# Performance work log

Measured on AMD Instinct MI355X. Metric: run time of the kernel, lower is better.

Reference implementation:

```python
import jax, jax.numpy as jnp
import numpy as np

B, S, HID = 1, 2048, 4096
H = 32
Q_LORA, KV_LORA = 1536, 512
NOPE, ROPE, VDIM = 128, 64, 128
EPS = 1e-6
ROPE_BASE = 10000.0


def rms_norm(x, w, eps=EPS):
    var = jnp.mean(x.astype(jnp.float32) ** 2, axis=-1, keepdims=True)
    return (x * jax.lax.rsqrt(var + eps)).astype(x.dtype) * w


def rope_cos_sin(position_ids, dim=ROPE):
    inv_freq = 1.0 / (ROPE_BASE ** (jnp.arange(0, dim, 2, dtype=jnp.float32) / dim))
    ang = position_ids.astype(jnp.float32)[..., None] * inv_freq  # [B,S,dim/2]
    return jnp.cos(ang), jnp.sin(ang)


def apply_rope(x, cos, sin):
    # x: [..., dim]; neox-style rotate_half on the rope slice
    d2 = x.shape[-1] // 2
    x1, x2 = x[..., :d2], x[..., d2:]
    return jnp.concatenate([x1 * cos - x2 * sin, x2 * cos + x1 * sin], axis=-1)


def setup_inputs() -> dict:
    key = jax.random.key(0)
    ks = jax.random.split(key, 8)
    s = 0.02
    return {
        "position_ids": jnp.broadcast_to(jnp.arange(S, dtype=jnp.int32), (B, S)),
        "hidden_states": jax.random.normal(ks[0], (B, S, HID), jnp.float32),
        "w_fused_a": jax.random.normal(ks[1], (Q_LORA + KV_LORA + ROPE, HID), jnp.float32) * s,
        "q_a_ln_w": jnp.ones((Q_LORA,), jnp.float32),
        "kv_a_ln_w": jnp.ones((KV_LORA,), jnp.float32),
        "w_q_b": jax.random.normal(ks[2], (H * (NOPE + ROPE), Q_LORA), jnp.float32) * s,
        "w_kv_b": jax.random.normal(ks[3], (H * 2 * NOPE, KV_LORA), jnp.float32) * s,
        "w_o": jax.random.normal(ks[4], (HID, H * VDIM), jnp.float32) * s,
    }


def reference(position_ids, hidden_states, w_fused_a, q_a_ln_w, kv_a_ln_w, w_q_b, w_kv_b, w_o):
    # fused A projection: -> [q_lora | kv_lora | rope]
    a = jnp.einsum('bsh,oh->bso', hidden_states, w_fused_a)
    cq = rms_norm(a[..., :Q_LORA], q_a_ln_w)
    ckv = rms_norm(a[..., Q_LORA:Q_LORA + KV_LORA], kv_a_ln_w)
    k_pe = a[..., Q_LORA + KV_LORA:]  # [B,S,ROPE], shared across heads

    # Q up-projection, split nope/rope per head
    q = jnp.einsum('bsr,or->bso', cq, w_q_b).reshape(B, S, H, NOPE + ROPE)
    q_nope, q_pe = q[..., :NOPE], q[..., NOPE:]

    # KV up-projection: per head [k_nope | v]
    kv = jnp.einsum('bsr,or->bso', ckv, w_kv_b).reshape(B, S, H, 2 * NOPE)
    k_nope, v = kv[..., :NOPE], kv[..., NOPE:]

    # RoPE on the rope slices only
    cos, sin = rope_cos_sin(position_ids)  # [B,S,ROPE/2]
    q_pe = apply_rope(q_pe, cos[:, :, None, :], sin[:, :, None, :])
    k_pe = apply_rope(k_pe, cos, sin)

    qf = jnp.concatenate([q_nope, q_pe], axis=-1)  # [B,S,H,NOPE+ROPE]
    kf = jnp.concatenate([k_nope, jnp.broadcast_to(k_pe[:, :, None, :], (B, S, H, ROPE))], axis=-1)

    scale = 1.0 / np.sqrt(NOPE + ROPE)
    scores = jnp.einsum('bshd,bthd->bhst', qf, kf) * scale
    causal = jnp.tril(jnp.ones((S, S), dtype=bool))
    scores = jnp.where(causal, scores, jnp.finfo(scores.dtype).min)
    p = jax.nn.softmax(scores, axis=-1)
    attn = jnp.einsum('bhst,bthd->bshd', p, v).reshape(B, S, H * VDIM)
    return jnp.einsum('bsd,od->bso', attn, w_o)
```

## Files before the change

### kernel.cpp

```cpp
#include <hip/hip_runtime.h>
#include <cmath>

#define S_LEN 2048
#define HID 4096
#define NHEAD 32
#define Q_LORA 1536
#define KV_LORA 512
#define NOPE 128
#define ROPE_D 64
#define VDIM 128
#define QK_DIM 192
#define FUSED_N 2112
#define FUSED_NPAD 2304

typedef __attribute__((ext_vector_type(8))) short short8;
typedef __attribute__((ext_vector_type(4))) float floatx4;
typedef unsigned short ushort_t;

__device__ inline short f2bf(float f) {
    union { float f; unsigned u; } v; v.f = f;
    unsigned r = (v.u + 0x7fffu + ((v.u >> 16) & 1u)) >> 16;
    return (short)r;
}
__device__ inline float bf2f(ushort_t u) {
    union { unsigned u; float f; } v; v.u = ((unsigned)u) << 16; return v.f;
}

#define GLOAD16(g, l)                                                        \
    __builtin_amdgcn_global_load_lds(                                        \
        (const __attribute__((address_space(1))) unsigned int*)(g),          \
        (__attribute__((address_space(3))) unsigned int*)(l), 16, 0, 0)

__device__ inline short8 conv8(const float* s) {
    const float4* s4 = (const float4*)s;
    float4 a = s4[0], b = s4[1];
    short8 v;
    v[0] = f2bf(a.x); v[1] = f2bf(a.y); v[2] = f2bf(a.z); v[3] = f2bf(a.w);
    v[4] = f2bf(b.x); v[5] = f2bf(b.y); v[6] = f2bf(b.z); v[7] = f2bf(b.w);
    return v;
}

#define CE0 (S_LEN * HID)
#define CE1 (CE0 + FUSED_NPAD * HID)
#define CE2 (CE1 + NHEAD * QK_DIM * Q_LORA)
#define CE3 (CE2 + NHEAD * 256 * KV_LORA)

__global__ __launch_bounds__(256) void conv_all(
    const float* __restrict__ hs, const float* __restrict__ w_a,
    const float* __restrict__ w_qb, const float* __restrict__ w_kvb,
    ushort_t* __restrict__ hs_bf, ushort_t* __restrict__ w_a_bf,
    ushort_t* __restrict__ w_qb_bf, ushort_t* __restrict__ w_kvb_bf)
{
    int i = (blockIdx.x * 256 + threadIdx.x) * 8;
    if (i < CE0) {
        *(short8*)(hs_bf + i) = conv8(hs + i);
    } else if (i < CE1) {
        int j = i - CE0;
        short8 v;
        if (j < FUSED_N * HID) v = conv8(w_a + j);
        else                   v = (short8){0,0,0,0,0,0,0,0};
        *(short8*)(w_a_bf + j) = v;
    } else if (i < CE2) {
        int j = i - CE1;
        *(short8*)(w_qb_bf + j) = conv8(w_qb + j);
    } else if (i < CE3) {
        int j = i - CE2;
        *(short8*)(w_kvb_bf + j) = conv8(w_kvb + j);
    }
}

__global__ __launch_bounds__(256) void conv_bf16(
    const float* __restrict__ src, ushort_t* __restrict__ dst, int n)
{
    int i = (blockIdx.x * 256 + threadIdx.x) * 8;
    if (i >= n) return;
    *(short8*)(dst + i) = conv8(src + i);
}

__global__ __launch_bounds__(256) void reduce_add_f32(
    const float* __restrict__ p0, const float* __restrict__ p1,
    float* __restrict__ o, int n)
{
    int i = (blockIdx.x * 256 + threadIdx.x) * 4;
    if (i >= n) return;
    float4 a = *(const float4*)(p0 + i);
    float4 b = *(const float4*)(p1 + i);
    float4 c; c.x = a.x + b.x; c.y = a.y + b.y; c.z = a.z + b.z; c.w = a.w + b.w;
    *(float4*)(o + i) = c;
}

__device__ __forceinline__ void gemm_pipe_body(
    const ushort_t* __restrict__ A, int lda,
    const ushort_t* __restrict__ B, int ldb,
    int m0, int n0, int kbeg, int nst,
    short8* LDS, floatx4 (&acc)[8][4], int tid)
{
    const int lane = tid & 63;
    const int wave = tid >> 6;
    const int m    = lane & 15;
    const int quad = lane >> 4;
    const int wr   = wave >> 2;
    const int wc   = wave & 3;

    auto stage = [&](int k0, int buf) {
        short8* dst = &LDS[buf * 2048];
        #pragma unroll
        for (int r = 0; r < 2; ++r) {
            int i  = tid + r * 512;
            int mi = i & 15, qd = (i >> 4) & 3, rb = i >> 6;
            GLOAD16(A + (size_t)(m0 + rb * 16 + mi) * lda + k0 + qd * 8, dst + i);
            GLOAD16(B + (size_t)(n0 + rb * 16 + mi) * ldb + k0 + qd * 8, dst + 1024 + i);
        }
    };

    stage(kbeg, 0);
    stage(kbeg + 32, 1);

    for (int i = 0; i < nst; ++i) {
        if (i + 2 < nst) {
            stage(kbeg + (i + 2) * 32, (i + 2) % 3);
            asm volatile("s_waitcnt vmcnt(8)" ::: "memory");
        } else if (i + 1 < nst) {
            asm volatile("s_waitcnt vmcnt(4)" ::: "memory");
        } else {
            asm volatile("s_waitcnt vmcnt(0)" ::: "memory");
        }
        asm volatile("s_barrier" ::: "memory");

        const short8* As = &LDS[(i % 3) * 2048];
        const short8* Bs = As + 1024;
        short8 af[8], bfr[4];
        #pragma unroll
        for (int ii = 0; ii < 8; ++ii)
            af[ii] = As[((wr * 8 + ii) * 4 + quad) * 16 + m];
        #pragma unroll
        for (int j = 0; j < 4; ++j)
            bfr[j] = Bs[((wc * 4 + j) * 4 + quad) * 16 + m];

        __builtin_amdgcn_s_setprio(1);
        #pragma unroll
        for (int ri = 0; ri < 8; ++ri)
            #pragma unroll
            for (int ci = 0; ci < 4; ++ci)
                acc[ri][ci] = __builtin_amdgcn_mfma_f32_16x16x32_bf16(
                    af[ri], bfr[ci], acc[ri][ci], 0, 0, 0);
        __builtin_amdgcn_s_setprio(0);

        asm volatile("s_barrier" ::: "memory");
    }
}

__device__ inline void store_c(float* p, float v)    { *p = v; }
__device__ inline void store_c(ushort_t* p, float v) { *p = (ushort_t)f2bf(v); }

template <typename CT>
__device__ __forceinline__ void gemm256_store(
    CT* __restrict__ C, int ldc, int N, int m0, int n0,
    floatx4 (&acc)[8][4], int tid)
{
    const int lane = tid & 63;
    const int wave = tid >> 6;
    const int m    = lane & 15;
    const int quad = lane >> 4;
    const int wr   = wave >> 2, wc = wave & 3;
    #pragma unroll
    for (int ci = 0; ci < 4; ++ci) {
        int col = n0 + wc * 64 + ci * 16 + m;
        if (col < N) {
            #pragma unroll
            for (int ri = 0; ri < 8; ++ri) {
                int row = m0 + wr * 128 + ri * 16 + quad * 4;
                #pragma unroll
                for (int r = 0; r < 4; ++r)
                    store_c(&C[(size_t)(row + r) * ldc + col], acc[ri][ci][r]);
            }
        }
    }
}

template <typename CT>
__global__ __launch_bounds__(512) void gemm256p(
    const ushort_t* __restrict__ A, int lda,
    const ushort_t* __restrict__ B, int ldb,
    CT* __restrict__ C, int ldc, int N, int Klen, int nx, int ny)
{
    __shared__ short8 LDS[3 * 2048];
    const int tid = threadIdx.x;

    const int nwg = gridDim.x;
    const int bid = blockIdx.x;
    const int wg  = (bid & 7) * (nwg >> 3) + (bid >> 3);
    const int nxy = nx * ny;
    const int z   = wg / nxy;
    const int rxy = wg - z * nxy;
    const int m0  = (rxy / nx) * 256;
    const int n0  = (rxy % nx) * 256;
    CT* Cz = C + (size_t)z * (size_t)ny * 256 * ldc;

    floatx4 acc[8][4];
    #pragma unroll
    for (int i = 0; i < 8; ++i)
        #pragma unroll
        for (int j = 0; j < 4; ++j) acc[i][j] = (floatx4){0.f, 0.f, 0.f, 0.f};

    gemm_pipe_body(A, lda, B, ldb, m0, n0, z * Klen, Klen >> 5, LDS, acc, tid);
    gemm256_store<CT>(Cz, ldc, N, m0, n0, acc, tid);
}

__global__ __launch_bounds__(512) void gemm34p(
    const ushort_t* __restrict__ a_bf,
    const ushort_t* __restrict__ w_qb_bf,
    const ushort_t* __restrict__ w_kvb_bf,
    ushort_t* __restrict__ q_bf,
    ushort_t* __restrict__ kv_bf)
{
    __shared__ short8 LDS[3 * 2048];
    const int tid = threadIdx.x;

    const int nwg = gridDim.x;
    const int bid = blockIdx.x;
    const int wg  = (bid & 7) * (nwg >> 3) + (bid >> 3);
    const int x   = wg % 56;
    const int m0  = (wg / 56) * 256;

    const ushort_t* A; const ushort_t* B; ushort_t* C;
    int ldb, ldc, N, K, n0;
    if (x < 24) {
        A = a_bf;            B = w_qb_bf;  C = q_bf;
        ldb = Q_LORA;        ldc = NHEAD * QK_DIM; N = NHEAD * QK_DIM;
        K = Q_LORA;          n0 = x * 256;
    } else {
        A = a_bf + Q_LORA;   B = w_kvb_bf; C = kv_bf;
        ldb = KV_LORA;       ldc = NHEAD * 256;    N = NHEAD * 256;
        K = KV_LORA;         n0 = (x - 24) * 256;
    }

    floatx4 acc[8][4];
    #pragma unroll
    for (int i = 0; i < 8; ++i)
        #pragma unroll
        for (int j = 0; j < 4; ++j) acc[i][j] = (floatx4){0.f, 0.f, 0.f, 0.f};

    gemm_pipe_body(A, FUSED_N, B, ldb, m0, n0, 0, K >> 5, LDS, acc, tid);
    gemm256_store<ushort_t>(C, ldc, N, m0, n0, acc, tid);
}

__global__ __launch_bounds__(256) void norm_rope_kernel(
    const float* __restrict__ part,
    ushort_t* __restrict__ a,
    const float* __restrict__ q_ln_w,
    const float* __restrict__ kv_ln_w,
    const int* __restrict__ pos_ids)
{
    const int s = blockIdx.x;
    const size_t PL = (size_t)S_LEN * FUSED_N;
    const float* r0 = part + (size_t)s * FUSED_N;
    ushort_t* row = a + (size_t)s * FUSED_N;
    __shared__ float red[256];
    const int tid = threadIdx.x;

    float vq[6];
    float ss = 0.f;
    #pragma unroll
    for (int j = 0; j < 6; ++j) {
        int i = tid + j * 256;
        vq[j] = (r0[i] + r0[i + PL]) + (r0[i + 2 * PL] + r0[i + 3 * PL]);
        ss += vq[j] * vq[j];
    }
    red[tid] = ss;
    __syncthreads();
    for (int w = 128; w > 0; w >>= 1) {
        if (tid < w) red[tid] += red[tid + w];
        __syncthreads();
    }
    float scale_q = rsqrtf(red[0] / (float)Q_LORA + 1e-6f);
    #pragma unroll
    for (int j = 0; j < 6; ++j) {
        int i = tid + j * 256;
        row[i] = (ushort_t)f2bf(vq[j] * scale_q * q_ln_w[i]);
    }
    __syncthreads();

    float vk[2];
    ss = 0.f;
    #pragma unroll
    for (int j = 0; j < 2; ++j) {
        int iw = tid + j * 256;
        int i  = Q_LORA + iw;
        vk[j] = (r0[i] + r0[i + PL]) + (r0[i + 2 * PL] + r0[i + 3 * PL]);
        ss += vk[j] * vk[j];
    }
    red[tid] = ss;
    __syncthreads();
    for (int w = 128; w > 0; w >>= 1) {
        if (tid < w) red[tid] += red[tid + w];
        __syncthreads();
    }
    float scale_kv = rsqrtf(red[0] / (float)KV_LORA + 1e-6f);
    #pragma unroll
    for (int j = 0; j < 2; ++j) {
        int iw = tid + j * 256;
        row[Q_LORA + iw] = (ushort_t)f2bf(vk[j] * scale_kv * kv_ln_w[iw]);
    }

    if (tid < 32) {
        const int j = tid;
        float pos = (float)pos_ids[s];
        float inv_freq = expf(-(float)j * (9.210340371976184f / 32.f));
        float ang = pos * inv_freq;
        float c = cosf(ang), sn = sinf(ang);
        int i1 = Q_LORA + KV_LORA + j;
        int i2 = i1 + 32;
        float x1 = (r0[i1] + r0[i1 + PL]) + (r0[i1 + 2 * PL] + r0[i1 + 3 * PL]);
        float x2 = (r0[i2] + r0[i2 + PL]) + (r0[i2 + 2 * PL] + r0[i2 + 3 * PL]);
        row[i1] = (ushort_t)f2bf(x1 * c - x2 * sn);
        row[i2] = (ushort_t)f2bf(x2 * c + x1 * sn);
    }
}

__global__ __launch_bounds__(256) void rope_q_kernel(
    ushort_t* __restrict__ q, const int* __restrict__ pos_ids)
{
    int idx = blockIdx.x * blockDim.x + threadIdx.x;
    if (idx >= S_LEN * NHEAD) return;
    int s = idx >> 5;
    float pos = (float)pos_ids[s];
    ushort_t* qp = q + (size_t)idx * QK_DIM + NOPE;
    #pragma unroll 4
    for (int j = 0; j < 32; ++j) {
        float inv_freq = expf(-(float)j * (9.210340371976184f / 32.f));
        float ang = pos * inv_freq;
        float c = cosf(ang), sn = sinf(ang);
        float x1 = bf2f(qp[j]), x2 = bf2f(qp[32 + j]);
        qp[j]      = (ushort_t)f2bf(x1 * c - x2 * sn);
        qp[32 + j] = (ushort_t)f2bf(x2 * c + x1 * sn);
    }
}

__global__ __launch_bounds__(256) void transpose_v(
    const ushort_t* __restrict__ kv, ushort_t* __restrict__ vt)
{
    __shared__ ushort_t vs[32][128];
    const int tid = threadIdx.x;
    const int h   = blockIdx.y;
    const int kb  = blockIdx.x;

    #pragma unroll
    for (int rep = 0; rep < 2; ++rep) {
        int i = rep * 256 + tid;
        int key = i >> 4, ch = i & 15;
        *(short8*)&vs[key][ch * 8] =
            *(const short8*)(kv + ((size_t)(kb * 32 + key) * NHEAD + h) * 256 + 128 + ch * 8);
    }
    __syncthreads();
    #pragma unroll
    for (int rep = 0; rep < 2; ++rep) {
        int i = rep * 256 + tid;
        int kq = i >> 7, d = i & 127;
        short8 v;
        #pragma unroll
        for (int j = 0; j < 8; ++j) v[j] = vs[kq * 8 + j][d];
        *(short8*)(vt + (((size_t)h * (S_LEN / 8) + kb * 4 + kq) * 128 + d) * 8) = v;
    }
}

__global__ __launch_bounds__(256) void attn_mfma(
    const ushort_t* __restrict__ q,
    const ushort_t* __restrict__ kv,
    const ushort_t* __restrict__ abuf,
    const ushort_t* __restrict__ vt,
    ushort_t* __restrict__ attn)
{
    __shared__ short8 KF[2][768];
    __shared__ short8 VF[2][512];
    __shared__ short8 PA[256];

    const int tid  = threadIdx.x;
    const int wave = tid >> 6;
    const int lane = tid & 63;
    const int m    = lane & 15;
    const int quad = lane >> 4;
    const int h    = blockIdx.y;
    const int pair = blockIdx.x;
    const int qtiles[2] = { 31 - pair, pair };

    const float scale = 0.07216878364870323f;
    short* pas = (short*)PA;

    auto stage_kv = [&](int t0, int buf) {
        #pragma unroll
        for (int rep = 0; rep < 3; ++rep) {
            int i   = rep * 256 + tid;
            int key = i & 31, qd = (i >> 5) & 3, c = i >> 7;
            if (c < 4)
                GLOAD16(kv + ((size_t)(t0 + key) * NHEAD + h) * 256 + c * 32 + qd * 8,
                        &KF[buf][i]);
            else
                GLOAD16(abuf + (size_t)(t0 + key) * FUSED_N + 2048 + (c - 4) * 32 + qd * 8,
                        &KF[buf][i]);
        }
        const ushort_t* vsrc = vt + ((size_t)h * (S_LEN / 8) + (t0 >> 3)) * 1024;
        GLOAD16(vsrc + (size_t)tid * 8, &VF[buf][tid]);
        GLOAD16(vsrc + (size_t)(256 + tid) * 8, &VF[buf][256 + tid]);
    };

    for (int qi = 0; qi < 2; ++qi) {
        const int q0 = qtiles[qi] * 64;
        const int qrow_base = q0 + wave * 16;

        short8 qf[6];
        {
            const ushort_t* qrow = q + ((size_t)(qrow_base + m) * NHEAD + h) * QK_DIM;
            #pragma unroll
            for (int c = 0; c < 6; ++c)
                qf[c] = *(const short8*)(qrow + c * 32 + quad * 8);
        }

        floatx4 O[8];
        #pragma unroll
        for (int t = 0; t < 8; ++t) O[t] = (floatx4){0.f, 0.f, 0.f, 0.f};
        float mrow[4] = {-1e30f, -1e30f, -1e30f, -1e30f};
        float lrow[4] = {0.f, 0.f, 0.f, 0.f};

        const int ntile = (q0 + 64) / 32;

        stage_kv(0, 0);
        __syncthreads();
        int cur = 0;

        for (int tt = 0; tt < ntile; ++tt) {
            const int t0 = tt * 32;
            if (tt + 1 < ntile) stage_kv(t0 + 32, cur ^ 1);

            floatx4 s0 = (floatx4){0.f, 0.f, 0.f, 0.f};
            floatx4 s1 = (floatx4){0.f, 0.f, 0.f, 0.f};
            const int kb = quad * 32 + m;
            __builtin_amdgcn_s_setprio(1);
            #pragma unroll
            for (int c = 0; c < 6; ++c) {
                s0 = __builtin_amdgcn_mfma_f32_16x16x32_bf16(qf[c], KF[cur][c * 128 + kb],      s0, 0, 0, 0);
                s1 = __builtin_amdgcn_mfma_f32_16x16x32_bf16(qf[c], KF[cur][c * 128 + kb + 16], s1, 0, 0, 0);
            }
            __builtin_amdgcn_s_setprio(0);

            const int qb = qrow_base + quad * 4;
            float sv0[4], sv1[4];
            #pragma unroll
            for (int r = 0; r < 4; ++r) {
                float a0 = s0[r] * scale;
                float a1 = s1[r] * scale;
                if (t0 + m > qb + r)      a0 = -1e30f;
                if (t0 + 16 + m > qb + r) a1 = -1e30f;
                sv0[r] = a0; sv1[r] = a1;
            }
            #pragma unroll
            for (int r = 0; r < 4; ++r) {
                float v = fmaxf(sv0[r], sv1[r]);
                v = fmaxf(v, __shfl_xor(v, 1));
                v = fmaxf(v, __shfl_xor(v, 2));
                v = fmaxf(v, __shfl_xor(v, 4));
                v = fmaxf(v, __shfl_xor(v, 8));
                if (v > mrow[r] + 8.f) {
                    float alpha = __expf(mrow[r] - v);
                    lrow[r] *= alpha;
                    #pragma unroll
                    for (int t = 0; t < 8; ++t) O[t][r] *= alpha;
                    mrow[r] = v;
                }
                float p0 = __expf(sv0[r] - mrow[r]);
                float p1 = __expf(sv1[r] - mrow[r]);
                lrow[r] += p0 + p1;
                int row = quad * 4 + r;
                short* pw = pas + wave * 512;
                pw[((m >> 3) + 0) * 128 + row * 8 + (m & 7)] = f2bf(p0);
                pw[((m >> 3) + 2) * 128 + row * 8 + (m & 7)] = f2bf(p1);
            }

            short8 pfrag = PA[wave * 64 + quad * 16 + m];
            __builtin_amdgcn_s_setprio(1);
            #pragma unroll
            for (int t = 0; t < 8; ++t) {
                O[t] = __builtin_amdgcn_mfma_f32_16x16x32_bf16(
                    pfrag, VF[cur][quad * 128 + m + 16 * t], O[t], 0, 0, 0);
            }
            __builtin_amdgcn_s_setprio(0);

            __syncthreads();
            cur ^= 1;
        }

        #pragma unroll
        for (int r = 0; r < 4; ++r) {
            float l = lrow[r];
            l += __shfl_xor(l, 1);
            l += __shfl_xor(l, 2);
            l += __shfl_xor(l, 4);
            l += __shfl_xor(l, 8);
            float linv = 1.f / l;
            int row = qrow_base + quad * 4 + r;
            ushort_t* dst = attn + ((size_t)row * NHEAD + h) * VDIM + m;
            #pragma unroll
            for (int t = 0; t < 8; ++t)
                dst[16 * t] = (ushort_t)f2bf(O[t][r] * linv);
        }
    }
}

extern "C" void kernel_launch(void* const* d_in, const int* in_sizes, int n_in,
                              void* d_out, int out_size, void* d_ws, size_t ws_size,
                              hipStream_t stream)
{
    const int*   pos    = (const int*)d_in[0];
    const float* hs     = (const float*)d_in[1];
    const float* w_a    = (const float*)d_in[2];
    const float* qlnw   = (const float*)d_in[3];
    const float* kvlnw  = (const float*)d_in[4];
    const float* w_qb   = (const float*)d_in[5];
    const float* w_kvb  = (const float*)d_in[6];
    const float* w_o    = (const float*)d_in[7];
    float* out = (float*)d_out;

    char* p = (char*)d_ws;
    ushort_t* a_bf    = (ushort_t*)p; p += (size_t)S_LEN * FUSED_N * 2;
    ushort_t* q_bf    = (ushort_t*)p; p += (size_t)S_LEN * NHEAD * QK_DIM * 2;
    ushort_t* kv_bf   = (ushort_t*)p; p += (size_t)S_LEN * NHEAD * 256 * 2;
    ushort_t* attn_bf = (ushort_t*)p; p += (size_t)S_LEN * HID * 2;
    ushort_t* hs_bf   = (ushort_t*)p; p += (size_t)S_LEN * HID * 2;
    ushort_t* w_a_bf  = (ushort_t*)p; p += (size_t)FUSED_NPAD * HID * 2;
    ushort_t* w_qb_bf = (ushort_t*)p; p += (size_t)NHEAD * QK_DIM * Q_LORA * 2;
    ushort_t* w_kvb_bf= (ushort_t*)p; p += (size_t)NHEAD * 256 * KV_LORA * 2;
    ushort_t* w_o_bf  = hs_bf;
    ushort_t* vt_bf   = w_qb_bf;
    float* part1 = (float*)q_bf;
    float* part7 = (float*)a_bf;

    if (ws_size < (size_t)(p - (char*)d_ws)) return;

    dim3 blk(256);
    dim3 blk512(512);
    auto cgrid = [](size_t n) { return dim3((unsigned)((n / 8 + 255) / 256)); };

    conv_all<<<dim3(CE3 / 2048), blk, 0, stream>>>(
        hs, w_a, w_qb, w_kvb, hs_bf, w_a_bf, w_qb_bf, w_kvb_bf);

    gemm256p<float><<<dim3((FUSED_NPAD / 256) * (S_LEN / 256) * 4), blk512, 0, stream>>>(
        hs_bf, HID, w_a_bf, HID, part1, FUSED_N, FUSED_N, HID / 4,
        FUSED_NPAD / 256, S_LEN / 256);

    conv_bf16<<<cgrid((size_t)HID * HID), blk, 0, stream>>>(w_o, w_o_bf, HID * HID);

    norm_rope_kernel<<<S_LEN, 256, 0, stream>>>(part1, a_bf, qlnw, kvlnw, pos);

    gemm34p<<<dim3(56 * (S_LEN / 256)), blk512, 0, stream>>>(
        a_bf, w_qb_bf, w_kvb_bf, q_bf, kv_bf);

    transpose_v<<<dim3(S_LEN / 32, NHEAD), blk, 0, stream>>>(kv_bf, vt_bf);

    rope_q_kernel<<<(S_LEN * NHEAD + 255) / 256, 256, 0, stream>>>(q_bf, pos);

    attn_mfma<<<dim3(16, NHEAD), blk, 0, stream>>>(
        q_bf, kv_bf, a_bf, vt_bf, attn_bf);

    gemm256p<float><<<dim3((HID / 256) * (S_LEN / 256) * 2), blk512, 0, stream>>>(
        attn_bf, HID, w_o_bf, HID, part7, HID, HID, HID / 2,
        HID / 256, S_LEN / 256);
    reduce_add_f32<<<cgrid((size_t)S_LEN * HID * 2), blk, 0, stream>>>(
        part7, part7 + (size_t)S_LEN * HID, out, S_LEN * HID);
}
```

Measured before the change: 647.5 us.

## Triple-buffer KV staging with vmcnt waits and exp2-based wave-uniform softmax

Deepens the K/V shared-memory pipeline from two to three buffers, prefetching two tiles ahead and using explicit s_waitcnt vmcnt counts with raw s_barrier in place of __syncthreads. The softmax folds log2(e) into the scale so it can use exp2f, and skips the cross-lane max shuffles when every lane in the wave stays within the lazy-rescale threshold. The aim is to hide global-load latency and trim per-tile softmax ALU work. The cost is more LDS, which may lower occupancy, and hand-counted vmcnt values that become fragile if the number of loads issued by stage_kv ever changes.

```diff
diff --git a/kernel.cpp b/kernel.cpp
--- a/kernel.cpp
+++ b/kernel.cpp
@@ -371,8 +371,8 @@
     const ushort_t* __restrict__ vt,
     ushort_t* __restrict__ attn)
 {
-    __shared__ short8 KF[2][768];
-    __shared__ short8 VF[2][512];
+    __shared__ short8 KF[3][768];
+    __shared__ short8 VF[3][512];
     __shared__ short8 PA[256];
 
     const int tid  = threadIdx.x;
@@ -384,7 +384,7 @@
     const int pair = blockIdx.x;
     const int qtiles[2] = { 31 - pair, pair };
 
-    const float scale = 0.07216878364870323f;
+    const float scale2 = 0.07216878364870323f * 1.4426950408889634f;
     short* pas = (short*)PA;
 
     auto stage_kv = [&](int t0, int buf) {
@@ -425,12 +425,20 @@
         const int ntile = (q0 + 64) / 32;
 
         stage_kv(0, 0);
-        __syncthreads();
-        int cur = 0;
+        stage_kv(32, 1);
 
         for (int tt = 0; tt < ntile; ++tt) {
             const int t0 = tt * 32;
-            if (tt + 1 < ntile) stage_kv(t0 + 32, cur ^ 1);
+            if (tt + 2 < ntile) {
+                stage_kv(t0 + 64, (tt + 2) % 3);
+                asm volatile("s_waitcnt vmcnt(10)" ::: "memory");
+            } else if (tt + 1 < ntile) {
+                asm volatile("s_waitcnt vmcnt(5)" ::: "memory");
+            } else {
+                asm volatile("s_waitcnt vmcnt(0)" ::: "memory");
+            }
+            asm volatile("s_barrier" ::: "memory");
+            const int cur = tt % 3;
 
             floatx4 s0 = (floatx4){0.f, 0.f, 0.f, 0.f};
             floatx4 s1 = (floatx4){0.f, 0.f, 0.f, 0.f};
@@ -447,8 +455,8 @@
             float sv0[4], sv1[4];
             #pragma unroll
             for (int r = 0; r < 4; ++r) {
-                float a0 = s0[r] * scale;
-                float a1 = s1[r] * scale;
+                float a0 = s0[r] * scale2;
+                float a1 = s1[r] * scale2;
                 if (t0 + m > qb + r)      a0 = -1e30f;
                 if (t0 + 16 + m > qb + r) a1 = -1e30f;
                 sv0[r] = a0; sv1[r] = a1;
@@ -456,19 +464,20 @@
             #pragma unroll
             for (int r = 0; r < 4; ++r) {
                 float v = fmaxf(sv0[r], sv1[r]);
-                v = fmaxf(v, __shfl_xor(v, 1));
-                v = fmaxf(v, __shfl_xor(v, 2));
-                v = fmaxf(v, __shfl_xor(v, 4));
-                v = fmaxf(v, __shfl_xor(v, 8));
-                if (v > mrow[r] + 8.f) {
-                    float alpha = __expf(mrow[r] - v);
+                if (!__all(v <= mrow[r] + 8.f)) {
+                    v = fmaxf(v, __shfl_xor(v, 1));
+                    v = fmaxf(v, __shfl_xor(v, 2));
+                    v = fmaxf(v, __shfl_xor(v, 4));
+                    v = fmaxf(v, __shfl_xor(v, 8));
+                    float mnew  = fmaxf(mrow[r], v);
+                    float alpha = exp2f(mrow[r] - mnew);
                     lrow[r] *= alpha;
                     #pragma unroll
                     for (int t = 0; t < 8; ++t) O[t][r] *= alpha;
-                    mrow[r] = v;
+                    mrow[r] = mnew;
                 }
-                float p0 = __expf(sv0[r] - mrow[r]);
-                float p1 = __expf(sv1[r] - mrow[r]);
+                float p0 = exp2f(sv0[r] - mrow[r]);
+                float p1 = exp2f(sv1[r] - mrow[r]);
                 lrow[r] += p0 + p1;
                 int row = quad * 4 + r;
                 short* pw = pas + wave * 512;
@@ -485,8 +494,7 @@
             }
             __builtin_amdgcn_s_setprio(0);
 
-            __syncthreads();
-            cur ^= 1;
+            asm volatile("s_barrier" ::: "memory");
         }
 
         #pragma unroll
```

Result: faster. 622.8 us (-3.8%).
